# Optimization experiments

Measured on AMD Instinct MI355X. Metric: run time of the kernel, lower is better.

## Reference

```python
import jax, jax.numpy as jnp
import numpy as np

B = 256          # graphs per batch
NN = 400         # ROI nodes per graph (N*(N-1)/2 = 79800 = input_dim)
HID = [32, 64, 128]
KS = [200, 100, 50]   # nodes kept after each TopKPooling (ratio 0.5 each)
EPS = 1e-5


def setup_inputs() -> dict:
    key = jax.random.key(0)
    ks = jax.random.split(key, 20)
    # flattened strict upper triangle of a nonnegative FC matrix per sample
    data = jax.random.uniform(ks[0], (B, NN * (NN - 1) // 2), dtype=jnp.float32)
    inp = {"data": data}
    dims = [1] + HID
    for l in range(3):
        fan_in = dims[l]
        inp[f"W{l+1}"] = jax.random.normal(ks[1 + 5 * l], (dims[l], dims[l + 1]), jnp.float32) / np.sqrt(fan_in)
        inp[f"b{l+1}"] = jnp.zeros((dims[l + 1],), jnp.float32)
        inp[f"g{l+1}"] = jnp.ones((dims[l + 1],), jnp.float32)      # BN gamma
        inp[f"be{l+1}"] = jnp.zeros((dims[l + 1],), jnp.float32)    # BN beta
        inp[f"p{l+1}"] = jax.random.normal(ks[4 + 5 * l], (dims[l + 1],), jnp.float32) * 0.1  # TopK score vector
    return inp


def _gcn_conv(A, X, W, b):
    # GCNConv with edge weights: add self loops (weight 1), symmetric D^-1/2 A D^-1/2
    n = A.shape[1]
    Al = A + jnp.eye(n, dtype=A.dtype)[None]          # (B, n, n)
    deg = Al.sum(axis=-1)                             # (B, n)
    dis = jnp.where(deg > 0, jax.lax.rsqrt(deg), 0.0)
    An = dis[:, :, None] * Al * dis[:, None, :]
    return jnp.einsum('bij,bjf->bif', An, X @ W) + b


def _block(A, X, W, b, g, be, p, k):
    # GCNConv -> ReLU -> BatchNorm(train stats) -> (dropout=identity) -> TopKPooling
    h = jax.nn.relu(_gcn_conv(A, X, W, b))
    mu = h.mean(axis=(0, 1))
    var = h.var(axis=(0, 1))
    h = (h - mu) * jax.lax.rsqrt(var + EPS) * g + be
    # TopKPooling: score = x . p / ||p||, keep top k per graph, gate by tanh(score)
    score = h @ p / jnp.linalg.norm(p)                # (B, n)
    vals, idx = jax.lax.top_k(score, k)               # (B, k)
    Xn = jnp.take_along_axis(h, idx[:, :, None], axis=1) * jnp.tanh(vals)[:, :, None]
    bi = jnp.arange(A.shape[0])[:, None, None]
    An = A[bi, idx[:, :, None], idx[:, None, :]]      # filter_adj: edges among kept nodes
    return An, Xn


def reference(data, W1, b1, g1, be1, p1, W2, b2, g2, be2, p2, W3, b3, g3, be3, p3):
    Bn = data.shape[0]
    iu0, iu1 = np.triu_indices(NN, 1)
    A = jnp.zeros((Bn, NN, NN), data.dtype).at[:, iu0, iu1].set(data)
    A = A + jnp.swapaxes(A, 1, 2)                     # symmetric FC adjacency, zero diag
    X = jnp.ones((Bn, NN, 1), data.dtype)             # initial node feature dim = 1
    A, X = _block(A, X, W1, b1, g1, be1, p1, KS[0])
    A, X = _block(A, X, W2, b2, g2, be2, p2, KS[1])
    A, X = _block(A, X, W3, b3, g3, be3, p3, KS[2])
    return X.max(axis=1)                              # global_max_pool -> (B, 128)
```

## Files before the change

### kernel.cpp

```cpp
#include <hip/hip_runtime.h>
#include <math.h>

#define BB   256
#define NN0  400
#define NE   79800
#define EPSF 1e-5f

__device__ __forceinline__ int tri_e(int a, int c) {
  return a*(NN0-1) - ((a*(a-1))>>1) + (c - a - 1);
}

__device__ __forceinline__ size_t PRI(int b, int ti, int tj, int r) {
  return (((size_t)b*7 + ti)*7 + tj)*64 + r;
}

__device__ __forceinline__ float wave_sum(float v) {
  #pragma unroll
  for (int o = 32; o > 0; o >>= 1) v += __shfl_xor(v, o, 64);
  return v;
}

__device__ __forceinline__ float rdlane(float v, int k) {
  return __int_as_float(__builtin_amdgcn_readlane(__float_as_int(v), k));
}

__device__ __forceinline__ void bitonic_desc(float* sc, int* si, int P) {
  const int tid = threadIdx.x;
  const int nt = blockDim.x;
  for (int k = 2; k <= P; k <<= 1) {
    for (int j = k >> 1; j > 0; j >>= 1) {
      __syncthreads();
      for (int i = tid; i < P; i += nt) {
        int ixj = i ^ j;
        if (ixj > i) {
          float a = sc[i], c = sc[ixj];
          int ai = si[i], ci = si[ixj];
          bool bef = (a > c) || (a == c && ai < ci);
          bool sw = ((i & k) == 0) ? !bef : bef;
          if (sw) { sc[i] = c; sc[ixj] = a; si[i] = ci; si[ixj] = ai; }
        }
      }
    }
  }
  __syncthreads();
}

__global__ __launch_bounds__(256) void k_tri_mv(
    const float* __restrict__ data,
    const float* __restrict__ pr_in, const float* __restrict__ pc_in,
    float* __restrict__ pr, float* __restrict__ pc) {
  __shared__ float tile[64][65];
  __shared__ float dI[64], dJ[64];
  const int xcd = blockIdx.x & 7, slot = blockIdx.x >> 3;
  const int b = xcd*32 + slot/7, q0 = slot % 7;
  const int tid = threadIdx.x;
  const int wave = tid >> 6, lane = tid & 63;
  const float* __restrict__ drow = data + (size_t)b*NE;
  int ti_a[4], tj_a[4];
  #pragma unroll
  for (int u = 0; u < 4; ++u) {
    int t = q0 + u*7;
    int ti = 0, rem = t;
    while (rem >= 7 - ti) { rem -= 7 - ti; ++ti; }
    ti_a[u] = ti; tj_a[u] = ti + rem;
  }
  float vreg[16];
  float rI = 0.f, rJ = 0.f;
  auto issue = [&](int u) {
    const int i0 = ti_a[u]*64, j0 = tj_a[u]*64;
    const int ni = min(64, NN0 - i0), nj = min(64, NN0 - j0);
    #pragma unroll
    for (int k = 0; k < 16; ++k) {
      const int rr = wave*16 + k;
      const int i = i0 + rr, j = j0 + lane;
      vreg[k] = 0.f;
      if (rr < ni && lane < nj && j > i) vreg[k] = drow[tri_e(i, j)];
    }
    if (pr_in) {
      if (tid < 64) {
        float a = 0.f;
        if (tid < ni) {
          const int tt = ti_a[u], r = tid;
          float acc = 1.f;
          for (int tj = tt; tj < 7; ++tj) acc += pr_in[PRI(b, tt, tj, r)];
          for (int ts = 0; ts <= tt; ++ts) acc += pc_in[PRI(b, ts, tt, r)];
          a = rsqrtf(acc);
        }
        rI = a;
      } else if (tid < 128) {
        const int c = tid - 64;
        float a = 0.f;
        if (c < nj) {
          const int tt = tj_a[u], r = c;
          float acc = 1.f;
          for (int tj = tt; tj < 7; ++tj) acc += pr_in[PRI(b, tt, tj, r)];
          for (int ts = 0; ts <= tt; ++ts) acc += pc_in[PRI(b, ts, tt, r)];
          a = rsqrtf(acc);
        }
        rJ = a;
      }
    } else {
      if (tid < 64) rI = (tid < ni) ? 1.f : 0.f;
      else if (tid < 128) rJ = (tid - 64 < nj) ? 1.f : 0.f;
    }
  };
  issue(0);
  #pragma unroll 1
  for (int u = 0; u < 4; ++u) {
    const int ti = ti_a[u], tj = tj_a[u];
    if (u) __syncthreads();
    #pragma unroll
    for (int k = 0; k < 16; ++k) tile[wave*16 + k][lane] = vreg[k];
    if (tid < 64) dI[tid] = rI;
    else if (tid < 128) dJ[tid-64] = rJ;
    __syncthreads();
    if (u + 1 < 4) issue(u + 1);
    {
      const int r = tid >> 2, q = tid & 3;
      float s = 0.f;
      #pragma unroll
      for (int c = 0; c < 16; ++c) s += tile[r][q*16 + c] * dJ[q*16 + c];
      s += __shfl_xor(s, 1, 64);
      s += __shfl_xor(s, 2, 64);
      if (q == 0) pr[PRI(b, ti, tj, r)] = s;
    }
    {
      const int c = tid >> 2, q = tid & 3;
      float s = 0.f;
      #pragma unroll
      for (int r = 0; r < 16; ++r) s += tile[q*16 + r][c] * dI[q*16 + r];
      s += __shfl_xor(s, 1, 64);
      s += __shfl_xor(s, 2, 64);
      if (q == 0) pc[PRI(b, ti, tj, c)] = s;
    }
  }
}

__global__ __launch_bounds__(256) void k_sfin_stats_red(
    const float* __restrict__ pr, const float* __restrict__ pc,
    const float* __restrict__ pr2, const float* __restrict__ pc2,
    const float* __restrict__ W1, const float* __restrict__ b1,
    float* __restrict__ s1, float* __restrict__ acc1) {
  __shared__ float sl[256];
  __shared__ float st[64];
  __shared__ float w1s[32], b1s[32];
  const int tid = threadIdx.x;
  const int i = blockIdx.x*256 + tid;
  if (tid < 32) { w1s[tid] = W1[tid]; b1s[tid] = b1[tid]; }
  if (tid < 64) st[tid] = 0.f;
  const int b = i / NN0, n = i % NN0;
  const int t = n >> 6, r = n & 63;
  float dacc = 1.f, sacc = 0.f;
  for (int tj = t; tj < 7; ++tj) { dacc += pr[PRI(b, t, tj, r)]; sacc += pr2[PRI(b, t, tj, r)]; }
  for (int ti = 0; ti <= t; ++ti) { dacc += pc[PRI(b, ti, t, r)]; sacc += pc2[PRI(b, ti, t, r)]; }
  const float d = rsqrtf(dacc);
  const float s = d * (d + sacc);
  s1[i] = s;
  sl[tid] = s;
  __syncthreads();
  const int f = tid & 31, sub = tid >> 5;
  const float w = w1s[f], bb = b1s[f];
  float S = 0.f, Q = 0.f;
  #pragma unroll
  for (int k = 0; k < 32; ++k) {
    const float ss = sl[sub*32 + k];
    const float h = fmaxf(ss*w + bb, 0.f);
    S += h; Q += h*h;
  }
  atomicAdd(&st[f], S);
  atomicAdd(&st[32+f], Q);
  __syncthreads();
  if (tid < 64) atomicAdd(&acc1[tid], st[tid]);
}

__global__ __launch_bounds__(512) void k_top1(
    const float* __restrict__ s1, const float* __restrict__ acc1,
    const float* __restrict__ W1, const float* __restrict__ b1,
    const float* __restrict__ g1, const float* __restrict__ be1,
    const float* __restrict__ p1, const float* __restrict__ W2,
    int* __restrict__ nodes2, int* __restrict__ sperm2, float* __restrict__ Y2) {
  __shared__ float sc[512]; __shared__ int si[512];
  __shared__ float sS[NN0];
  __shared__ float tvs[200];
  __shared__ int nds_l[200];
  __shared__ float w1s[32], b1s[32], cfs[32], scs[32], shs[32];
  __shared__ __align__(16) float hp[6400];
  __shared__ float c0s;
  const int tid = threadIdx.x;
  const int b = (blockIdx.x & 7)*32 + (blockIdx.x >> 3);
  if (tid < 32) { w1s[tid] = W1[tid]; b1s[tid] = b1[tid]; }
  if (tid < 64) {
    float scale = 0.f, shift = 0.f, pv = 0.f;
    if (tid < 32) {
      const float S = acc1[tid], Q = acc1[32 + tid];
      const float N = 102400.f;
      const float mu = S / N;
      const float var = Q / N - mu*mu;
      const float inv = rsqrtf(var + EPSF);
      scale = inv * g1[tid];
      shift = be1[tid] - mu * scale;
      pv = p1[tid];
    }
    const float pn = sqrtf(wave_sum(pv*pv));
    if (tid < 32) { scs[tid] = scale; shs[tid] = shift; cfs[tid] = scale*pv/pn; }
    float u = (tid < 32) ? shift*pv/pn : 0.f;
    u = wave_sum(u);
    if (tid == 0) c0s = u;
  }
  __syncthreads();
  const float c0 = c0s;
  {
    const int i = tid;
    if (i < NN0) {
      const float s = s1[(size_t)b*NN0 + i];
      sS[i] = s;
      float sco = c0;
      #pragma unroll
      for (int f = 0; f < 32; ++f) sco += fmaxf(s*w1s[f] + b1s[f], 0.f) * cfs[f];
      sc[i] = sco; si[i] = i;
    } else { sc[i] = -INFINITY; si[i] = 0x7fffffff; }
  }
  bitonic_desc(sc, si, 512);
  for (int k = tid; k < 200; k += 512) {
    tvs[k] = tanhf(sc[k]);
    nds_l[k] = si[k];
    nodes2[b*200 + k] = si[k];
  }
  __syncthreads();
  for (int o = tid; o < 6400; o += 512) {
    const int k = o >> 5, f = o & 31;
    const float s = sS[nds_l[k]];
    const float h = fmaxf(s*w1s[f] + b1s[f], 0.f);
    hp[o] = (h*scs[f] + shs[f]) * tvs[k];
  }
  __syncthreads();
  {
    const int g = tid & 63;
    float wr[32];
    #pragma unroll
    for (int f = 0; f < 32; ++f) wr[f] = W2[f*64 + g];
    for (int o = tid; o < 12800; o += 512) {
      const int k = o >> 6;
      float acc = 0.f;
      #pragma unroll
      for (int c4 = 0; c4 < 8; ++c4) {
        const float4 x4 = *(const float4*)&hp[(k<<5) + (c4<<2)];
        acc += x4.x*wr[c4*4] + x4.y*wr[c4*4+1] + x4.z*wr[c4*4+2] + x4.w*wr[c4*4+3];
      }
      Y2[(size_t)b*12800 + o] = acc;
    }
  }
  __syncthreads();
  if (tid < 256) {
    sc[tid] = (tid < 200) ? -(float)nds_l[tid] : -INFINITY;
    si[tid] = (tid < 200) ? tid : 0x7fffffff;
  }
  bitonic_desc(sc, si, 256);
  if (tid < 200) sperm2[b*200 + tid] = si[tid];
}

__global__ __launch_bounds__(256) void k_gatherA2(
    const float* __restrict__ data, const int* __restrict__ nodes2,
    const int* __restrict__ sperm2, float* __restrict__ A2, float* __restrict__ dis2) {
  __shared__ int nds[200], sp[200], sn[200];
  __shared__ float rowbuf[4][200];
  const int idx = blockIdx.x;
  const int r9 = idx >> 3;
  const int b = (idx & 7)*32 + r9/50;
  const int rg = r9 % 50;
  const int tid = threadIdx.x;
  if (tid < 200) { nds[tid] = nodes2[b*200 + tid]; sp[tid] = sperm2[b*200 + tid]; }
  __syncthreads();
  if (tid < 200) sn[tid] = nds[sp[tid]];
  __syncthreads();
  const int wave = tid >> 6, lane = tid & 63;
  const int i = rg*4 + wave;
  const int ni = nds[i];
  const float* __restrict__ drow = data + (size_t)b*NE;
  float accd = 0.f;
  for (int jj = lane; jj < 200; jj += 64) {
    const int sj = sn[jj];
    float v = 0.f;
    if (sj != ni) {
      const int a = min(ni, sj), c = max(ni, sj);
      v = drow[tri_e(a, c)];
    }
    rowbuf[wave][sp[jj]] = v;
    accd += v;
  }
  __syncthreads();
  for (int j = lane; j < 200; j += 64)
    A2[((size_t)b*200 + i)*200 + j] = rowbuf[wave][j];
  accd = wave_sum(accd);
  if (lane == 0) dis2[b*200 + i] = rsqrtf(1.f + accd);
}

__global__ __launch_bounds__(256) void k_conv2(
    const float* __restrict__ A2, const float* __restrict__ Y2,
    const float* __restrict__ dis2, const float* __restrict__ b2,
    float* __restrict__ h2g, float* __restrict__ acc2g) {
  __shared__ __align__(16) float zb[200*64];
  __shared__ float dsb[200];
  __shared__ float st[128];
  const int tid = threadIdx.x;
  const int xcd = blockIdx.x & 7, slot = blockIdx.x >> 3;
  const int b = xcd*32 + (slot >> 1), p = slot & 1;
  const int wave = tid >> 6, lane = tid & 63;
  if (tid < 128) st[tid] = 0.f;
  if (tid < 200) dsb[tid] = dis2[b*200 + tid];
  for (int t = tid; t < 3200; t += 256) {
    const int row = t >> 4, f4 = t & 15;
    const float dz = dis2[b*200 + row];
    float4 v = *(const float4*)&Y2[((size_t)b*200 + row)*64 + (f4 << 2)];
    v.x *= dz; v.y *= dz; v.z *= dz; v.w *= dz;
    *(float4*)&zb[(row << 6) + (f4 << 2)] = v;
  }
  const float bl = b2[lane];
  __syncthreads();
  const int rb = p*100 + wave*25;
  auto ldA = [&](int j) -> float {
    return (lane < 25) ? A2[((size_t)b*200 + j)*200 + rb + lane] : 0.f;
  };
  float acc[25];
  #pragma unroll
  for (int k = 0; k < 25; ++k) acc[k] = 0.f;
  float a_cur = ldA(0);
  #pragma unroll 2
  for (int j = 0; j < 200; ++j) {
    const float a_nxt = (j < 199) ? ldA(j + 1) : 0.f;
    const float z = zb[(j << 6) + lane];
    #pragma unroll
    for (int k = 0; k < 25; ++k)
      acc[k] = fmaf(rdlane(a_cur, k), z, acc[k]);
    a_cur = a_nxt;
  }
  float ss = 0.f, qq = 0.f;
  #pragma unroll
  for (int k = 0; k < 25; ++k) {
    const int r = rb + k;
    const float d = dsb[r];
    const float h = fmaxf(d*(acc[k] + zb[(r << 6) + lane]) + bl, 0.f);
    h2g[((size_t)b*200 + r)*64 + lane] = h;
    ss += h; qq += h*h;
  }
  atomicAdd(&st[lane], ss);
  atomicAdd(&st[64 + lane], qq);
  __syncthreads();
  if (tid < 128) atomicAdd(&acc2g[tid], st[tid]);
}

__global__ __launch_bounds__(512) void k_top2(
    const float* __restrict__ h2g, const float* __restrict__ acc2,
    const float* __restrict__ g2, const float* __restrict__ be2,
    const float* __restrict__ p2, const float* __restrict__ W3,
    const int* __restrict__ nodes2, int* __restrict__ nodes3,
    float* __restrict__ Y3) {
  __shared__ float sc[256]; __shared__ int si[256];
  __shared__ __align__(16) float xs[6400];
  __shared__ float sc2[64], sh2[64], cf2[64];
  __shared__ float c20s;
  const int tid = threadIdx.x;
  const int b = (blockIdx.x & 7)*32 + (blockIdx.x >> 3);
  if (tid < 64) {
    const float S = acc2[tid], Q = acc2[64 + tid];
    const float N = 51200.f;
    const float mu = S/N, var = Q/N - mu*mu, inv = rsqrtf(var + EPSF);
    const float scale = inv*g2[tid], shift = be2[tid] - mu*scale;
    const float pv = p2[tid];
    const float pn = sqrtf(wave_sum(pv*pv));
    sc2[tid] = scale; sh2[tid] = shift; cf2[tid] = scale*pv/pn;
    const float u = wave_sum(shift*pv/pn);
    if (tid == 0) c20s = u;
  }
  __syncthreads();
  const int wave = tid >> 6, lane = tid & 63;
  const float cf = cf2[lane];
  const float c20 = c20s;
  for (int i = wave; i < 200; i += 8) {
    float v = h2g[((size_t)b*200 + i)*64 + lane] * cf;
    v = wave_sum(v);
    if (lane == 0) { sc[i] = v + c20; si[i] = i; }
  }
  if (tid >= 200 && tid < 256) { sc[tid] = -INFINITY; si[tid] = 0x7fffffff; }
  bitonic_desc(sc, si, 256);
  const float scale = sc2[lane], shift = sh2[lane];
  for (int o = tid; o < 6400; o += 512) {
    const int k = o >> 6;
    const int idx = si[k];
    const float tv = tanhf(sc[k]);
    xs[o] = (h2g[((size_t)b*200 + idx)*64 + lane] * scale + shift) * tv;
  }
  for (int k = tid; k < 100; k += 512) nodes3[b*100 + k] = nodes2[b*200 + si[k]];
  __syncthreads();
  {
    const int g = tid & 127;
    float wr[64];
    #pragma unroll
    for (int f = 0; f < 64; ++f) wr[f] = W3[f*128 + g];
    for (int o = tid; o < 12800; o += 512) {
      const int k = o >> 7;
      float acc = 0.f;
      #pragma unroll
      for (int c4 = 0; c4 < 16; ++c4) {
        const float4 x4 = *(const float4*)&xs[(k<<6) + (c4<<2)];
        acc += x4.x*wr[c4*4] + x4.y*wr[c4*4+1] + x4.z*wr[c4*4+2] + x4.w*wr[c4*4+3];
      }
      Y3[(size_t)b*12800 + o] = acc;
    }
  }
}

__global__ __launch_bounds__(256) void k_gatherA3(
    const float* __restrict__ data, const int* __restrict__ nodes3,
    float* __restrict__ A3, float* __restrict__ dis3) {
  __shared__ int nds[100];
  const int slot = blockIdx.x >> 3;
  const int b = (blockIdx.x & 7)*32 + slot/25, rg = slot % 25;
  const int tid = threadIdx.x;
  if (tid < 100) nds[tid] = nodes3[b*100 + tid];
  __syncthreads();
  const int wave = tid >> 6, lane = tid & 63;
  const int i = rg*4 + wave;
  const int ni = nds[i];
  const float* __restrict__ drow = data + (size_t)b*NE;
  float accd = 0.f;
  for (int j = lane; j < 100; j += 64) {
    float v = 0.f;
    if (j != i) {
      const int nj = nds[j];
      const int a = min(ni, nj), c = max(ni, nj);
      v = drow[tri_e(a, c)];
    }
    A3[((size_t)b*100 + i)*100 + j] = v;
    accd += v;
  }
  accd = wave_sum(accd);
  if (lane == 0) dis3[b*100 + i] = rsqrtf(1.f + accd);
}

__global__ __launch_bounds__(256) void k_conv3(
    const float* __restrict__ A3, const float* __restrict__ Y3,
    const float* __restrict__ dis3, const float* __restrict__ b3,
    float* __restrict__ h3g, float* __restrict__ acc3g) {
  __shared__ __align__(16) float zb[100*128];
  __shared__ float dsb[100];
  __shared__ float st[256];
  const int tid = threadIdx.x;
  const int xcd = blockIdx.x & 7, slot = blockIdx.x >> 3;
  const int b = xcd*32 + (slot >> 1), p = slot & 1;
  const int wave = tid >> 6, lane = tid & 63;
  st[tid] = 0.f;
  if (tid < 100) dsb[tid] = dis3[b*100 + tid];
  for (int t = tid; t < 3200; t += 256) {
    const int row = t >> 5, f4 = t & 31;
    const float dz = dis3[b*100 + row];
    float4 v = *(const float4*)&Y3[((size_t)b*100 + row)*128 + (f4 << 2)];
    v.x *= dz; v.y *= dz; v.z *= dz; v.w *= dz;
    *(float4*)&zb[(row << 7) + (f4 << 2)] = v;
  }
  const float bl0 = b3[lane], bl1 = b3[64 + lane];
  __syncthreads();
  const int rb = p*50;
  const int lw = wave*13;
  auto ldA = [&](int j) -> float {
    return (lane < 13 && lw + lane < 50)
      ? A3[((size_t)b*100 + j)*100 + rb + lw + lane] : 0.f;
  };
  float acc0[13], acc1[13];
  #pragma unroll
  for (int k = 0; k < 13; ++k) { acc0[k] = 0.f; acc1[k] = 0.f; }
  float a_cur = ldA(0);
  #pragma unroll 2
  for (int j = 0; j < 100; ++j) {
    const float a_nxt = (j < 99) ? ldA(j + 1) : 0.f;
    const float z0 = zb[(j << 7) + lane];
    const float z1 = zb[(j << 7) + 64 + lane];
    #pragma unroll
    for (int k = 0; k < 13; ++k) {
      const float av = rdlane(a_cur, k);
      acc0[k] = fmaf(av, z0, acc0[k]);
      acc1[k] = fmaf(av, z1, acc1[k]);
    }
    a_cur = a_nxt;
  }
  float ss0 = 0.f, qq0 = 0.f, ss1 = 0.f, qq1 = 0.f;
  #pragma unroll
  for (int k = 0; k < 13; ++k) {
    const int lr = lw + k;
    if (lr < 50) {
      const int r = rb + lr;
      const float d = dsb[r];
      const float h0 = fmaxf(d*(acc0[k] + zb[(r << 7) + lane]) + bl0, 0.f);
      const float h1 = fmaxf(d*(acc1[k] + zb[(r << 7) + 64 + lane]) + bl1, 0.f);
      h3g[((size_t)b*100 + r)*128 + lane] = h0;
      h3g[((size_t)b*100 + r)*128 + 64 + lane] = h1;
      ss0 += h0; qq0 += h0*h0; ss1 += h1; qq1 += h1*h1;
    }
  }
  atomicAdd(&st[lane], ss0);
  atomicAdd(&st[64 + lane], ss1);
  atomicAdd(&st[128 + lane], qq0);
  atomicAdd(&st[192 + lane], qq1);
  __syncthreads();
  atomicAdd(&acc3g[tid], st[tid]);
}

__global__ __launch_bounds__(256) void k_top3(
    const float* __restrict__ h3g, const float* __restrict__ acc3,
    const float* __restrict__ g3, const float* __restrict__ be3,
    const float* __restrict__ p3, float* __restrict__ out) {
  __shared__ float sc[128]; __shared__ int si[128]; __shared__ float tv[64];
  __shared__ float scl[128], shl[128], cfl[128];
  __shared__ float red2[4];
  const int tid = threadIdx.x;
  const int b = (blockIdx.x & 7)*32 + (blockIdx.x >> 3);
  const int wave = tid >> 6, lane = tid & 63;
  float scale = 0.f, shift = 0.f, pv = 0.f;
  if (tid < 128) {
    const float S = acc3[tid], Q = acc3[128 + tid];
    const float N = 25600.f;
    const float mu = S/N, var = Q/N - mu*mu, inv = rsqrtf(var + EPSF);
    scale = inv*g3[tid]; shift = be3[tid] - mu*scale; pv = p3[tid];
    const float t2 = wave_sum(pv*pv);
    if (lane == 0) red2[wave] = t2;
  }
  __syncthreads();
  const float pn = sqrtf(red2[0] + red2[1]);
  if (tid < 128) {
    scl[tid] = scale; shl[tid] = shift; cfl[tid] = scale*pv/pn;
    const float u = wave_sum(shift*pv/pn);
    if (lane == 0) red2[2 + wave] = u;
  }
  __syncthreads();
  const float c30 = red2[2] + red2[3];
  const float clo = cfl[lane], chi = cfl[64 + lane];
  for (int i = wave; i < 100; i += 4) {
    const float* hr = h3g + ((size_t)b*100 + i)*128;
    float v = hr[lane]*clo + hr[64 + lane]*chi;
    v = wave_sum(v);
    if (lane == 0) { sc[i] = v + c30; si[i] = i; }
  }
  if (tid >= 100 && tid < 128) { sc[tid] = -INFINITY; si[tid] = 0x7fffffff; }
  bitonic_desc(sc, si, 128);
  if (tid < 50) tv[tid] = tanhf(sc[tid]);
  __syncthreads();
  if (tid < 128) {
    const float scalev = scl[tid], shiftv = shl[tid];
    float m = -INFINITY;
    for (int k = 0; k < 50; ++k) {
      const float h = h3g[((size_t)b*100 + si[k])*128 + tid];
      m = fmaxf(m, (h*scalev + shiftv)*tv[k]);
    }
    out[(size_t)b*128 + tid] = m;
  }
}

extern "C" void kernel_launch(void* const* d_in, const int* in_sizes, int n_in,
                              void* d_out, int out_size, void* d_ws, size_t ws_size,
                              hipStream_t stream) {
  (void)in_sizes; (void)n_in; (void)out_size; (void)ws_size;
  const float* data = (const float*)d_in[0];
  const float* W1 = (const float*)d_in[1];
  const float* b1 = (const float*)d_in[2];
  const float* g1 = (const float*)d_in[3];
  const float* be1 = (const float*)d_in[4];
  const float* p1 = (const float*)d_in[5];
  const float* W2 = (const float*)d_in[6];
  const float* b2 = (const float*)d_in[7];
  const float* g2 = (const float*)d_in[8];
  const float* be2 = (const float*)d_in[9];
  const float* p2 = (const float*)d_in[10];
  const float* W3 = (const float*)d_in[11];
  const float* b3 = (const float*)d_in[12];
  const float* g3 = (const float*)d_in[13];
  const float* be3 = (const float*)d_in[14];
  const float* p3 = (const float*)d_in[15];
  float* out = (float*)d_out;

  char* ws = (char*)d_ws;
  size_t off = 0;
  auto alloc = [&](size_t n) { size_t o = off; off += (n + 255) & ~(size_t)255; return o; };
  float* pr     = (float*)(ws + alloc((size_t)BB*49*64*4));
  float* pc     = (float*)(ws + alloc((size_t)BB*49*64*4));
  float* pr2    = (float*)(ws + alloc((size_t)BB*49*64*4));
  float* pc2    = (float*)(ws + alloc((size_t)BB*49*64*4));
  float* s1     = (float*)(ws + alloc((size_t)BB*NN0*4));
  float* accz   = (float*)(ws + alloc(448*4));
  int*   nodes2 = (int*)  (ws + alloc((size_t)BB*200*4));
  int*   sperm2 = (int*)  (ws + alloc((size_t)BB*200*4));
  float* Y2     = (float*)(ws + alloc((size_t)BB*12800*4));
  float* A2     = (float*)(ws + alloc((size_t)BB*40000*4));
  float* dis2   = (float*)(ws + alloc((size_t)BB*200*4));
  float* h2     = (float*)(ws + alloc((size_t)BB*12800*4));
  int*   nodes3 = (int*)  (ws + alloc((size_t)BB*100*4));
  float* Y3     = (float*)(ws + alloc((size_t)BB*12800*4));
  float* A3     = (float*)(ws + alloc((size_t)BB*10000*4));
  float* dis3   = (float*)(ws + alloc((size_t)BB*100*4));
  float* h3     = (float*)(ws + alloc((size_t)BB*12800*4));
  float* acc1 = accz;
  float* acc2 = accz + 64;
  float* acc3 = accz + 192;

  hipMemsetAsync(accz, 0, 448*4, stream);
  k_tri_mv<<<dim3(BB*7), dim3(256), 0, stream>>>(data, nullptr, nullptr, pr, pc);
  k_tri_mv<<<dim3(BB*7), dim3(256), 0, stream>>>(data, pr, pc, pr2, pc2);
  k_sfin_stats_red<<<dim3(400), dim3(256), 0, stream>>>(pr, pc, pr2, pc2, W1, b1, s1, acc1);
  k_top1<<<dim3(BB), dim3(512), 0, stream>>>(s1, acc1, W1, b1, g1, be1, p1, W2, nodes2, sperm2, Y2);
  k_gatherA2<<<dim3(BB*50), dim3(256), 0, stream>>>(data, nodes2, sperm2, A2, dis2);
  k_conv2<<<dim3(BB*2), dim3(256), 0, stream>>>(A2, Y2, dis2, b2, h2, acc2);
  k_top2<<<dim3(BB), dim3(512), 0, stream>>>(h2, acc2, g2, be2, p2, W3, nodes2, nodes3, Y3);
  k_gatherA3<<<dim3(BB*25), dim3(256), 0, stream>>>(data, nodes3, A3, dis3);
  k_conv3<<<dim3(BB*2), dim3(256), 0, stream>>>(A3, Y3, dis3, b3, h3, acc3);
  k_top3<<<dim3(BB), dim3(256), 0, stream>>>(h3, acc3, g3, be3, p3, out);
}
```

Before: 433.1 us.

## Fold row degree scaling into A, drop LDS staging, split conv into quarters

The gather kernels now multiply each adjacency row by its own rsqrt degree before storing it, so the conv kernels no longer need to pre-scale Y into a large shared buffer. The conv2/conv3 kernels drop that LDS tile and read Y straight from global memory with register double-buffering. Each graph is split across four blocks instead of two, and each load of A fetches four rows at once across lanes, broadcast with readlane. The goal is higher occupancy and no LDS staging cost, at the price of more redundant global reads of Y across blocks and slightly different rounding from the changed order of the degree scaling.

```diff
diff --git a/kernel.cpp b/kernel.cpp
--- a/kernel.cpp
+++ b/kernel.cpp
@@ -289,59 +289,94 @@
     accd += v;
   }
   __syncthreads();
+  accd = wave_sum(accd);
+  const float dd = rsqrtf(1.f + accd);
   for (int j = lane; j < 200; j += 64)
-    A2[((size_t)b*200 + i)*200 + j] = rowbuf[wave][j];
-  accd = wave_sum(accd);
-  if (lane == 0) dis2[b*200 + i] = rsqrtf(1.f + accd);
+    A2[((size_t)b*200 + i)*200 + j] = rowbuf[wave][j] * dd;
+  if (lane == 0) dis2[b*200 + i] = dd;
 }
 
 __global__ __launch_bounds__(256) void k_conv2(
     const float* __restrict__ A2, const float* __restrict__ Y2,
     const float* __restrict__ dis2, const float* __restrict__ b2,
     float* __restrict__ h2g, float* __restrict__ acc2g) {
-  __shared__ __align__(16) float zb[200*64];
   __shared__ float dsb[200];
   __shared__ float st[128];
   const int tid = threadIdx.x;
   const int xcd = blockIdx.x & 7, slot = blockIdx.x >> 3;
-  const int b = xcd*32 + (slot >> 1), p = slot & 1;
+  const int b = xcd*32 + (slot >> 2), p = slot & 3;
   const int wave = tid >> 6, lane = tid & 63;
   if (tid < 128) st[tid] = 0.f;
   if (tid < 200) dsb[tid] = dis2[b*200 + tid];
-  for (int t = tid; t < 3200; t += 256) {
-    const int row = t >> 4, f4 = t & 15;
-    const float dz = dis2[b*200 + row];
-    float4 v = *(const float4*)&Y2[((size_t)b*200 + row)*64 + (f4 << 2)];
-    v.x *= dz; v.y *= dz; v.z *= dz; v.w *= dz;
-    *(float4*)&zb[(row << 6) + (f4 << 2)] = v;
-  }
+  __syncthreads();
   const float bl = b2[lane];
-  __syncthreads();
-  const int rb = p*100 + wave*25;
-  auto ldA = [&](int j) -> float {
-    return (lane < 25) ? A2[((size_t)b*200 + j)*200 + rb + lane] : 0.f;
+  const int rbl = p*50 + wave*13;
+  const int lq = lane / 13, lk = lane - lq*13;
+  const bool lv = (lane < 52) && (wave*13 + lk < 50);
+  const float* __restrict__ Ab = A2 + (size_t)b*40000;
+  const float* __restrict__ Yb = Y2 + (size_t)b*12800;
+  auto ldA = [&](int j4) -> float {
+    return lv ? Ab[(size_t)(j4 + lq)*200 + rbl + lk] : 0.f;
   };
-  float acc[25];
-  #pragma unroll
-  for (int k = 0; k < 25; ++k) acc[k] = 0.f;
-  float a_cur = ldA(0);
-  #pragma unroll 2
-  for (int j = 0; j < 200; ++j) {
-    const float a_nxt = (j < 199) ? ldA(j + 1) : 0.f;
-    const float z = zb[(j << 6) + lane];
-    #pragma unroll
-    for (int k = 0; k < 25; ++k)
-      acc[k] = fmaf(rdlane(a_cur, k), z, acc[k]);
-    a_cur = a_nxt;
+  float acc[13];
+  #pragma unroll
+  for (int k = 0; k < 13; ++k) acc[k] = 0.f;
+  float a0 = ldA(0), a1 = ldA(4);
+  float z0[4], z1[4];
+  #pragma unroll
+  for (int q = 0; q < 4; ++q) z0[q] = Yb[q*64 + lane];
+  #pragma unroll
+  for (int q = 0; q < 4; ++q) z1[q] = Yb[(4 + q)*64 + lane];
+  #pragma unroll 1
+  for (int it = 0; it < 25; ++it) {
+    const int j0 = it*8;
+    {
+      const float a = a0;
+      float z[4];
+      #pragma unroll
+      for (int q = 0; q < 4; ++q) z[q] = z0[q];
+      if (it < 24) {
+        a0 = ldA(j0 + 8);
+        #pragma unroll
+        for (int q = 0; q < 4; ++q) z0[q] = Yb[(j0 + 8 + q)*64 + lane];
+      }
+      #pragma unroll
+      for (int q = 0; q < 4; ++q) {
+        #pragma unroll
+        for (int k = 0; k < 13; ++k)
+          acc[k] = fmaf(rdlane(a, q*13 + k), z[q], acc[k]);
+      }
+    }
+    {
+      const float a = a1;
+      float z[4];
+      #pragma unroll
+      for (int q = 0; q < 4; ++q) z[q] = z1[q];
+      if (it < 24) {
+        a1 = ldA(j0 + 12);
+        #pragma unroll
+        for (int q = 0; q < 4; ++q) z1[q] = Yb[(j0 + 12 + q)*64 + lane];
+      }
+      #pragma unroll
+      for (int q = 0; q < 4; ++q) {
+        #pragma unroll
+        for (int k = 0; k < 13; ++k)
+          acc[k] = fmaf(rdlane(a, q*13 + k), z[q], acc[k]);
+      }
+    }
   }
   float ss = 0.f, qq = 0.f;
   #pragma unroll
-  for (int k = 0; k < 25; ++k) {
-    const int r = rb + k;
-    const float d = dsb[r];
-    const float h = fmaxf(d*(acc[k] + zb[(r << 6) + lane]) + bl, 0.f);
-    h2g[((size_t)b*200 + r)*64 + lane] = h;
-    ss += h; qq += h*h;
+  for (int k = 0; k < 13; ++k) {
+    const int lr = wave*13 + k;
+    if (lr < 50) {
+      const int r = p*50 + lr;
+      const float d = dsb[r];
+      const float y = Yb[(size_t)r*64 + lane];
+      const float h = fmaxf(d*acc[k] + d*(d*y) + bl, 0.f);
+      h2g[((size_t)b*200 + r)*64 + lane] = h;
+      ss += h; qq += h*h;
+    }
   }
   atomicAdd(&st[lane], ss);
   atomicAdd(&st[64 + lane], qq);
@@ -423,75 +458,128 @@
   const int i = rg*4 + wave;
   const int ni = nds[i];
   const float* __restrict__ drow = data + (size_t)b*NE;
-  float accd = 0.f;
-  for (int j = lane; j < 100; j += 64) {
-    float v = 0.f;
-    if (j != i) {
-      const int nj = nds[j];
-      const int a = min(ni, nj), c = max(ni, nj);
-      v = drow[tri_e(a, c)];
-    }
-    A3[((size_t)b*100 + i)*100 + j] = v;
-    accd += v;
-  }
-  accd = wave_sum(accd);
-  if (lane == 0) dis3[b*100 + i] = rsqrtf(1.f + accd);
+  const int j0 = lane, j1 = 64 + lane;
+  float v0 = 0.f, v1 = 0.f;
+  if (j0 != i) {
+    const int nj = nds[j0];
+    const int a = min(ni, nj), c = max(ni, nj);
+    v0 = drow[tri_e(a, c)];
+  }
+  if (j1 < 100 && j1 != i) {
+    const int nj = nds[j1];
+    const int a = min(ni, nj), c = max(ni, nj);
+    v1 = drow[tri_e(a, c)];
+  }
+  const float accd = wave_sum(v0 + v1);
+  const float dd = rsqrtf(1.f + accd);
+  A3[((size_t)b*100 + i)*100 + j0] = v0 * dd;
+  if (j1 < 100) A3[((size_t)b*100 + i)*100 + j1] = v1 * dd;
+  if (lane == 0) dis3[b*100 + i] = dd;
 }
 
 __global__ __launch_bounds__(256) void k_conv3(
     const float* __restrict__ A3, const float* __restrict__ Y3,
     const float* __restrict__ dis3, const float* __restrict__ b3,
     float* __restrict__ h3g, float* __restrict__ acc3g) {
-  __shared__ __align__(16) float zb[100*128];
   __shared__ float dsb[100];
   __shared__ float st[256];
   const int tid = threadIdx.x;
   const int xcd = blockIdx.x & 7, slot = blockIdx.x >> 3;
-  const int b = xcd*32 + (slot >> 1), p = slot & 1;
+  const int b = xcd*32 + (slot >> 2), p = slot & 3;
   const int wave = tid >> 6, lane = tid & 63;
   st[tid] = 0.f;
   if (tid < 100) dsb[tid] = dis3[b*100 + tid];
-  for (int t = tid; t < 3200; t += 256) {
-    const int row = t >> 5, f4 = t & 31;
-    const float dz = dis3[b*100 + row];
-    float4 v = *(const float4*)&Y3[((size_t)b*100 + row)*128 + (f4 << 2)];
-    v.x *= dz; v.y *= dz; v.z *= dz; v.w *= dz;
-    *(float4*)&zb[(row << 7) + (f4 << 2)] = v;
-  }
+  __syncthreads();
   const float bl0 = b3[lane], bl1 = b3[64 + lane];
-  __syncthreads();
-  const int rb = p*50;
-  const int lw = wave*13;
-  auto ldA = [&](int j) -> float {
-    return (lane < 13 && lw + lane < 50)
-      ? A3[((size_t)b*100 + j)*100 + rb + lw + lane] : 0.f;
+  const int rbl = p*25 + wave*7;
+  const int lq = lane / 7, lk = lane - lq*7;
+  const bool lv = (lq < 4) && (wave*7 + lk < 25);
+  const float* __restrict__ Ab = A3 + (size_t)b*10000;
+  const float* __restrict__ Yb = Y3 + (size_t)b*12800;
+  auto ldA = [&](int j4) -> float {
+    return lv ? Ab[(size_t)(j4 + lq)*100 + rbl + lk] : 0.f;
   };
-  float acc0[13], acc1[13];
-  #pragma unroll
-  for (int k = 0; k < 13; ++k) { acc0[k] = 0.f; acc1[k] = 0.f; }
-  float a_cur = ldA(0);
-  #pragma unroll 2
-  for (int j = 0; j < 100; ++j) {
-    const float a_nxt = (j < 99) ? ldA(j + 1) : 0.f;
-    const float z0 = zb[(j << 7) + lane];
-    const float z1 = zb[(j << 7) + 64 + lane];
+  float ac0[7], ac1[7];
+  #pragma unroll
+  for (int k = 0; k < 7; ++k) { ac0[k] = 0.f; ac1[k] = 0.f; }
+  float a0 = ldA(0), a1 = ldA(4);
+  float z0[8], z1[8];
+  #pragma unroll
+  for (int q = 0; q < 4; ++q) {
+    z0[2*q] = Yb[q*128 + lane];       z0[2*q+1] = Yb[q*128 + 64 + lane];
+    z1[2*q] = Yb[(4+q)*128 + lane];   z1[2*q+1] = Yb[(4+q)*128 + 64 + lane];
+  }
+  #pragma unroll 1
+  for (int it = 0; it < 12; ++it) {
+    const int j0 = it*8;
+    {
+      const float a = a0;
+      float z[8];
+      #pragma unroll
+      for (int q = 0; q < 8; ++q) z[q] = z0[q];
+      a0 = ldA(j0 + 8);
+      #pragma unroll
+      for (int q = 0; q < 4; ++q) {
+        z0[2*q]   = Yb[(j0 + 8 + q)*128 + lane];
+        z0[2*q+1] = Yb[(j0 + 8 + q)*128 + 64 + lane];
+      }
+      #pragma unroll
+      for (int q = 0; q < 4; ++q) {
+        #pragma unroll
+        for (int k = 0; k < 7; ++k) {
+          const float av = rdlane(a, q*7 + k);
+          ac0[k] = fmaf(av, z[2*q], ac0[k]);
+          ac1[k] = fmaf(av, z[2*q+1], ac1[k]);
+        }
+      }
+    }
+    {
+      const float a = a1;
+      float z[8];
+      #pragma unroll
+      for (int q = 0; q < 8; ++q) z[q] = z1[q];
+      if (it < 11) {
+        a1 = ldA(j0 + 12);
+        #pragma unroll
+        for (int q = 0; q < 4; ++q) {
+          z1[2*q]   = Yb[(j0 + 12 + q)*128 + lane];
+          z1[2*q+1] = Yb[(j0 + 12 + q)*128 + 64 + lane];
+        }
+      }
+      #pragma unroll
+      for (int q = 0; q < 4; ++q) {
+        #pragma unroll
+        for (int k = 0; k < 7; ++k) {
+          const float av = rdlane(a, q*7 + k);
+          ac0[k] = fmaf(av, z[2*q], ac0[k]);
+          ac1[k] = fmaf(av, z[2*q+1], ac1[k]);
+        }
+      }
+    }
+  }
+  {
+    const float a = a0;
     #pragma unroll
-    for (int k = 0; k < 13; ++k) {
-      const float av = rdlane(a_cur, k);
-      acc0[k] = fmaf(av, z0, acc0[k]);
-      acc1[k] = fmaf(av, z1, acc1[k]);
-    }
-    a_cur = a_nxt;
+    for (int q = 0; q < 4; ++q) {
+      #pragma unroll
+      for (int k = 0; k < 7; ++k) {
+        const float av = rdlane(a, q*7 + k);
+        ac0[k] = fmaf(av, z0[2*q], ac0[k]);
+        ac1[k] = fmaf(av, z0[2*q+1], ac1[k]);
+      }
+    }
   }
   float ss0 = 0.f, qq0 = 0.f, ss1 = 0.f, qq1 = 0.f;
   #pragma unroll
-  for (int k = 0; k < 13; ++k) {
-    const int lr = lw + k;
-    if (lr < 50) {
-      const int r = rb + lr;
+  for (int k = 0; k < 7; ++k) {
+    const int lr = wave*7 + k;
+    if (lr < 25) {
+      const int r = p*25 + lr;
       const float d = dsb[r];
-      const float h0 = fmaxf(d*(acc0[k] + zb[(r << 7) + lane]) + bl0, 0.f);
-      const float h1 = fmaxf(d*(acc1[k] + zb[(r << 7) + 64 + lane]) + bl1, 0.f);
+      const float y0 = Yb[(size_t)r*128 + lane];
+      const float y1 = Yb[(size_t)r*128 + 64 + lane];
+      const float h0 = fmaxf(d*ac0[k] + d*(d*y0) + bl0, 0.f);
+      const float h1 = fmaxf(d*ac1[k] + d*(d*y1) + bl1, 0.f);
       h3g[((size_t)b*100 + r)*128 + lane] = h0;
       h3g[((size_t)b*100 + r)*128 + 64 + lane] = h1;
       ss0 += h0; qq0 += h0*h0; ss1 += h1; qq1 += h1*h1;
@@ -607,9 +695,9 @@
   k_sfin_stats_red<<<dim3(400), dim3(256), 0, stream>>>(pr, pc, pr2, pc2, W1, b1, s1, acc1);
   k_top1<<<dim3(BB), dim3(512), 0, stream>>>(s1, acc1, W1, b1, g1, be1, p1, W2, nodes2, sperm2, Y2);
   k_gatherA2<<<dim3(BB*50), dim3(256), 0, stream>>>(data, nodes2, sperm2, A2, dis2);
-  k_conv2<<<dim3(BB*2), dim3(256), 0, stream>>>(A2, Y2, dis2, b2, h2, acc2);
+  k_conv2<<<dim3(BB*4), dim3(256), 0, stream>>>(A2, Y2, dis2, b2, h2, acc2);
   k_top2<<<dim3(BB), dim3(512), 0, stream>>>(h2, acc2, g2, be2, p2, W3, nodes2, nodes3, Y3);
   k_gatherA3<<<dim3(BB*25), dim3(256), 0, stream>>>(data, nodes3, A3, dis3);
-  k_conv3<<<dim3(BB*2), dim3(256), 0, stream>>>(A3, Y3, dis3, b3, h3, acc3);
+  k_conv3<<<dim3(BB*4), dim3(256), 0, stream>>>(A3, Y3, dis3, b3, h3, acc3);
   k_top3<<<dim3(BB), dim3(256), 0, stream>>>(h3, acc3, g3, be3, p3, out);
 }
```

New measurement: 419.0 us. -3.3%, faster.

## Split GCN conv2/conv3 across more blocks, fold column norm into gathered A

Applied to the files above, without the earlier changes.

The gather kernels now pre-scale each adjacency row by its own D^-1/2 factor. Because the adjacency is symmetric, this lets the conv kernels read Y straight from global memory and skip the LDS staging copy of dis-scaled Y. The conv kernels are split into 8 blocks per graph instead of 2, with fewer accumulators per thread, and each A load is reused across 8 or 16 source rows via readlane. This aims to raise occupancy and parallelism in the small per-graph matmuls. In exchange, Y is re-read from global memory or L2 by every block, with no LDS reuse, and the remainder handling adds complexity.

```diff
diff --git a/kernel.cpp b/kernel.cpp
--- a/kernel.cpp
+++ b/kernel.cpp
@@ -289,59 +289,64 @@
     accd += v;
   }
   __syncthreads();
+  accd = wave_sum(accd);
+  const float dd = rsqrtf(1.f + accd);
   for (int j = lane; j < 200; j += 64)
-    A2[((size_t)b*200 + i)*200 + j] = rowbuf[wave][j];
-  accd = wave_sum(accd);
-  if (lane == 0) dis2[b*200 + i] = rsqrtf(1.f + accd);
+    A2[((size_t)b*200 + i)*200 + j] = rowbuf[wave][j] * dd;
+  if (lane == 0) dis2[b*200 + i] = dd;
 }
 
 __global__ __launch_bounds__(256) void k_conv2(
     const float* __restrict__ A2, const float* __restrict__ Y2,
     const float* __restrict__ dis2, const float* __restrict__ b2,
     float* __restrict__ h2g, float* __restrict__ acc2g) {
-  __shared__ __align__(16) float zb[200*64];
   __shared__ float dsb[200];
   __shared__ float st[128];
   const int tid = threadIdx.x;
   const int xcd = blockIdx.x & 7, slot = blockIdx.x >> 3;
-  const int b = xcd*32 + (slot >> 1), p = slot & 1;
+  const int b = xcd*32 + (slot >> 3), p = slot & 7;
   const int wave = tid >> 6, lane = tid & 63;
   if (tid < 128) st[tid] = 0.f;
   if (tid < 200) dsb[tid] = dis2[b*200 + tid];
-  for (int t = tid; t < 3200; t += 256) {
-    const int row = t >> 4, f4 = t & 15;
-    const float dz = dis2[b*200 + row];
-    float4 v = *(const float4*)&Y2[((size_t)b*200 + row)*64 + (f4 << 2)];
-    v.x *= dz; v.y *= dz; v.z *= dz; v.w *= dz;
-    *(float4*)&zb[(row << 6) + (f4 << 2)] = v;
-  }
+  __syncthreads();
   const float bl = b2[lane];
-  __syncthreads();
-  const int rb = p*100 + wave*25;
-  auto ldA = [&](int j) -> float {
-    return (lane < 25) ? A2[((size_t)b*200 + j)*200 + rb + lane] : 0.f;
+  const int rbl = p*25 + wave*7;
+  const int lq = lane / 7, lk = lane - lq*7;
+  const bool lv = (lane < 56) && (wave*7 + lk < 25);
+  const float* __restrict__ Ab = A2 + (size_t)b*40000;
+  const float* __restrict__ Yb = Y2 + (size_t)b*12800;
+  auto ldA = [&](int j8) -> float {
+    return lv ? Ab[(size_t)(j8 + lq)*200 + rbl + lk] : 0.f;
   };
-  float acc[25];
+  float acc[7];
   #pragma unroll
-  for (int k = 0; k < 25; ++k) acc[k] = 0.f;
+  for (int k = 0; k < 7; ++k) acc[k] = 0.f;
   float a_cur = ldA(0);
-  #pragma unroll 2
-  for (int j = 0; j < 200; ++j) {
-    const float a_nxt = (j < 199) ? ldA(j + 1) : 0.f;
-    const float z = zb[(j << 6) + lane];
+  #pragma unroll 1
+  for (int jg = 0; jg < 25; ++jg) {
+    const float a = a_cur;
+    if (jg < 24) a_cur = ldA((jg + 1)*8);
+    const int j0 = jg*8;
     #pragma unroll
-    for (int k = 0; k < 25; ++k)
-      acc[k] = fmaf(rdlane(a_cur, k), z, acc[k]);
-    a_cur = a_nxt;
+    for (int q = 0; q < 8; ++q) {
+      const float z = Yb[(j0 + q)*64 + lane];
+      #pragma unroll
+      for (int k = 0; k < 7; ++k)
+        acc[k] = fmaf(rdlane(a, q*7 + k), z, acc[k]);
+    }
   }
   float ss = 0.f, qq = 0.f;
   #pragma unroll
-  for (int k = 0; k < 25; ++k) {
-    const int r = rb + k;
-    const float d = dsb[r];
-    const float h = fmaxf(d*(acc[k] + zb[(r << 6) + lane]) + bl, 0.f);
-    h2g[((size_t)b*200 + r)*64 + lane] = h;
-    ss += h; qq += h*h;
+  for (int k = 0; k < 7; ++k) {
+    const int lr = wave*7 + k;
+    if (lr < 25) {
+      const int r = p*25 + lr;
+      const float d = dsb[r];
+      const float y = Yb[(size_t)r*64 + lane];
+      const float h = fmaxf(d*acc[k] + d*(d*y) + bl, 0.f);
+      h2g[((size_t)b*200 + r)*64 + lane] = h;
+      ss += h; qq += h*h;
+    }
   }
   atomicAdd(&st[lane], ss);
   atomicAdd(&st[64 + lane], qq);
@@ -423,75 +428,96 @@
   const int i = rg*4 + wave;
   const int ni = nds[i];
   const float* __restrict__ drow = data + (size_t)b*NE;
-  float accd = 0.f;
-  for (int j = lane; j < 100; j += 64) {
-    float v = 0.f;
-    if (j != i) {
-      const int nj = nds[j];
-      const int a = min(ni, nj), c = max(ni, nj);
-      v = drow[tri_e(a, c)];
-    }
-    A3[((size_t)b*100 + i)*100 + j] = v;
-    accd += v;
-  }
-  accd = wave_sum(accd);
-  if (lane == 0) dis3[b*100 + i] = rsqrtf(1.f + accd);
+  const int j0 = lane, j1 = 64 + lane;
+  float v0 = 0.f, v1 = 0.f;
+  if (j0 != i) {
+    const int nj = nds[j0];
+    const int a = min(ni, nj), c = max(ni, nj);
+    v0 = drow[tri_e(a, c)];
+  }
+  if (j1 < 100 && j1 != i) {
+    const int nj = nds[j1];
+    const int a = min(ni, nj), c = max(ni, nj);
+    v1 = drow[tri_e(a, c)];
+  }
+  const float accd = wave_sum(v0 + v1);
+  const float dd = rsqrtf(1.f + accd);
+  A3[((size_t)b*100 + i)*100 + j0] = v0 * dd;
+  if (j1 < 100) A3[((size_t)b*100 + i)*100 + j1] = v1 * dd;
+  if (lane == 0) dis3[b*100 + i] = dd;
 }
 
 __global__ __launch_bounds__(256) void k_conv3(
     const float* __restrict__ A3, const float* __restrict__ Y3,
     const float* __restrict__ dis3, const float* __restrict__ b3,
     float* __restrict__ h3g, float* __restrict__ acc3g) {
-  __shared__ __align__(16) float zb[100*128];
   __shared__ float dsb[100];
   __shared__ float st[256];
   const int tid = threadIdx.x;
   const int xcd = blockIdx.x & 7, slot = blockIdx.x >> 3;
-  const int b = xcd*32 + (slot >> 1), p = slot & 1;
+  const int b = xcd*32 + (slot >> 3), p = slot & 7;
   const int wave = tid >> 6, lane = tid & 63;
   st[tid] = 0.f;
   if (tid < 100) dsb[tid] = dis3[b*100 + tid];
-  for (int t = tid; t < 3200; t += 256) {
-    const int row = t >> 5, f4 = t & 31;
-    const float dz = dis3[b*100 + row];
-    float4 v = *(const float4*)&Y3[((size_t)b*100 + row)*128 + (f4 << 2)];
-    v.x *= dz; v.y *= dz; v.z *= dz; v.w *= dz;
-    *(float4*)&zb[(row << 7) + (f4 << 2)] = v;
-  }
+  __syncthreads();
   const float bl0 = b3[lane], bl1 = b3[64 + lane];
-  __syncthreads();
-  const int rb = p*50;
-  const int lw = wave*13;
-  auto ldA = [&](int j) -> float {
-    return (lane < 13 && lw + lane < 50)
-      ? A3[((size_t)b*100 + j)*100 + rb + lw + lane] : 0.f;
+  const int rbl = p*13 + wave*4;
+  const int lq = lane >> 2, lk = lane & 3;
+  const bool lvr = (wave*4 + lk < 13) && (rbl + lk < 100);
+  const float* __restrict__ Ab = A3 + (size_t)b*10000;
+  const float* __restrict__ Yb = Y3 + (size_t)b*12800;
+  auto ldA = [&](int j16) -> float {
+    return lvr ? Ab[(size_t)(j16 + lq)*100 + rbl + lk] : 0.f;
   };
-  float acc0[13], acc1[13];
+  auto ldAt = [&](int j16) -> float {
+    return (lvr && lq < 4) ? Ab[(size_t)(j16 + lq)*100 + rbl + lk] : 0.f;
+  };
+  float ac0[4], ac1[4];
   #pragma unroll
-  for (int k = 0; k < 13; ++k) { acc0[k] = 0.f; acc1[k] = 0.f; }
+  for (int k = 0; k < 4; ++k) { ac0[k] = 0.f; ac1[k] = 0.f; }
   float a_cur = ldA(0);
-  #pragma unroll 2
-  for (int j = 0; j < 100; ++j) {
-    const float a_nxt = (j < 99) ? ldA(j + 1) : 0.f;
-    const float z0 = zb[(j << 7) + lane];
-    const float z1 = zb[(j << 7) + 64 + lane];
+  #pragma unroll 1
+  for (int jg = 0; jg < 6; ++jg) {
+    const float a = a_cur;
+    a_cur = (jg < 5) ? ldA((jg + 1)*16) : ldAt(96);
+    const int j0 = jg*16;
     #pragma unroll
-    for (int k = 0; k < 13; ++k) {
-      const float av = rdlane(a_cur, k);
-      acc0[k] = fmaf(av, z0, acc0[k]);
-      acc1[k] = fmaf(av, z1, acc1[k]);
-    }
-    a_cur = a_nxt;
+    for (int q = 0; q < 16; ++q) {
+      const float z0 = Yb[(j0 + q)*128 + lane];
+      const float z1 = Yb[(j0 + q)*128 + 64 + lane];
+      #pragma unroll
+      for (int k = 0; k < 4; ++k) {
+        const float av = rdlane(a, (q << 2) + k);
+        ac0[k] = fmaf(av, z0, ac0[k]);
+        ac1[k] = fmaf(av, z1, ac1[k]);
+      }
+    }
+  }
+  {
+    const float a = a_cur;
+    #pragma unroll
+    for (int q = 0; q < 4; ++q) {
+      const float z0 = Yb[(96 + q)*128 + lane];
+      const float z1 = Yb[(96 + q)*128 + 64 + lane];
+      #pragma unroll
+      for (int k = 0; k < 4; ++k) {
+        const float av = rdlane(a, (q << 2) + k);
+        ac0[k] = fmaf(av, z0, ac0[k]);
+        ac1[k] = fmaf(av, z1, ac1[k]);
+      }
+    }
   }
   float ss0 = 0.f, qq0 = 0.f, ss1 = 0.f, qq1 = 0.f;
   #pragma unroll
-  for (int k = 0; k < 13; ++k) {
-    const int lr = lw + k;
-    if (lr < 50) {
-      const int r = rb + lr;
+  for (int k = 0; k < 4; ++k) {
+    const int lr = wave*4 + k;
+    const int r = p*13 + lr;
+    if (lr < 13 && r < 100) {
       const float d = dsb[r];
-      const float h0 = fmaxf(d*(acc0[k] + zb[(r << 7) + lane]) + bl0, 0.f);
-      const float h1 = fmaxf(d*(acc1[k] + zb[(r << 7) + 64 + lane]) + bl1, 0.f);
+      const float y0 = Yb[(size_t)r*128 + lane];
+      const float y1 = Yb[(size_t)r*128 + 64 + lane];
+      const float h0 = fmaxf(d*ac0[k] + d*(d*y0) + bl0, 0.f);
+      const float h1 = fmaxf(d*ac1[k] + d*(d*y1) + bl1, 0.f);
       h3g[((size_t)b*100 + r)*128 + lane] = h0;
       h3g[((size_t)b*100 + r)*128 + 64 + lane] = h1;
       ss0 += h0; qq0 += h0*h0; ss1 += h1; qq1 += h1*h1;
@@ -607,9 +633,9 @@
   k_sfin_stats_red<<<dim3(400), dim3(256), 0, stream>>>(pr, pc, pr2, pc2, W1, b1, s1, acc1);
   k_top1<<<dim3(BB), dim3(512), 0, stream>>>(s1, acc1, W1, b1, g1, be1, p1, W2, nodes2, sperm2, Y2);
   k_gatherA2<<<dim3(BB*50), dim3(256), 0, stream>>>(data, nodes2, sperm2, A2, dis2);
-  k_conv2<<<dim3(BB*2), dim3(256), 0, stream>>>(A2, Y2, dis2, b2, h2, acc2);
+  k_conv2<<<dim3(BB*8), dim3(256), 0, stream>>>(A2, Y2, dis2, b2, h2, acc2);
   k_top2<<<dim3(BB), dim3(512), 0, stream>>>(h2, acc2, g2, be2, p2, W3, nodes2, nodes3, Y3);
   k_gatherA3<<<dim3(BB*25), dim3(256), 0, stream>>>(data, nodes3, A3, dis3);
-  k_conv3<<<dim3(BB*2), dim3(256), 0, stream>>>(A3, Y3, dis3, b3, h3, acc3);
+  k_conv3<<<dim3(BB*8), dim3(256), 0, stream>>>(A3, Y3, dis3, b3, h3, acc3);
   k_top3<<<dim3(BB), dim3(256), 0, stream>>>(h3, acc3, g3, be3, p3, out);
 }
```

Result: slower. 453.1 us (+4.6%).
